# Performance work log

Hardware: AMD Instinct MI355X
Metric: run time of the kernel (lower is better)

Reference implementation:

```python
import jax, jax.numpy as jnp
import numpy as np


def _pad_ones(x):
    # prepend a ones column: [B, d] -> [B, d+1]
    b = x.shape[0]
    return jnp.concatenate([jnp.ones((b, 1), dtype=x.dtype), x], axis=1)


def setup_inputs() -> dict:
    key = jax.random.key(0)
    kt, ka, kv = jax.random.split(key, 3)
    B, D = 128, 63
    return {
        "t": jax.random.normal(kt, (B, D), dtype=jnp.float32),
        "a": jax.random.normal(ka, (B, D), dtype=jnp.float32),
        "v": jax.random.normal(kv, (B, D), dtype=jnp.float32),
    }


def reference(t, a, v):
    # Faithful to: bmm(a1[:, :, None], v1[:, None, :]) -> [B, da+1, dv+1],
    # then reshape to [B, (da+1)(dv+1), 1] and bmm with t1[:, None, :],
    # then flatten. Equivalent to triple outer product with index order (a, v, t).
    ah = _pad_ones(a)   # [B, da+1]
    vh = _pad_ones(v)   # [B, dv+1]
    th = _pad_ones(t)   # [B, dt+1]
    fusion = jnp.einsum('bi,bj,bk->bijk', ah, vh, th)  # [B, da+1, dv+1, dt+1]
    return fusion.reshape(a.shape[0], -1)
```

## Files before the change

### kernel.cpp

```cpp
#include <hip/hip_runtime.h>


__global__ __launch_bounds__(256) void tensorFusion_kernel(
    const float* __restrict__ t,
    const float* __restrict__ a,
    const float* __restrict__ v,
    float* __restrict__ out)
{
    const int D = 63;
    const int bi = blockIdx.x;
    const int b  = bi >> 6;
    const int i  = bi & 63;

    __shared__ float vh[64];
    __shared__ float th[64];

    const int tid = threadIdx.x;
    if (tid < 64) {
        vh[tid] = (tid == 0) ? 1.0f : v[b * D + (tid - 1)];
        th[tid] = (tid == 0) ? 1.0f : t[b * D + (tid - 1)];
    }
    const float ai = (i == 0) ? 1.0f : a[b * D + (i - 1)];
    __syncthreads();

    float4* __restrict__ outp = reinterpret_cast<float4*>(out + (size_t)bi * 4096);

    #pragma unroll
    for (int pass = 0; pass < 4; ++pass) {
        const int idx = pass * 256 + tid;
        const int off = idx << 2;
        const int j   = off >> 6;
        const int k   = off & 63;
        const float s = ai * vh[j];
        float4 r;
        r.x = s * th[k + 0];
        r.y = s * th[k + 1];
        r.z = s * th[k + 2];
        r.w = s * th[k + 3];
        outp[idx] = r;
    }
}

extern "C" void kernel_launch(void* const* d_in, const int* in_sizes, int n_in,
                              void* d_out, int out_size, void* d_ws, size_t ws_size,
                              hipStream_t stream) {
    const float* t = (const float*)d_in[0];
    const float* a = (const float*)d_in[1];
    const float* v = (const float*)d_in[2];
    float* out = (float*)d_out;

    tensorFusion_kernel<<<dim3(128 * 64), dim3(256), 0, stream>>>(t, a, v, out);
}
```

Before: 25.95 us.

## Compute four a-rows per block with nontemporal vector stores

Each block now produces four consecutive i rows instead of one, so the grid shrinks fourfold and each shared-memory load of v and t is reused across four output rows. The t values are read as 128-bit vectors from shared memory, and outputs are written with nontemporal stores to avoid cache pollution on this write-only, 16 MB output. Fewer blocks reduce launch and setup overhead, though there is less parallelism to hide store latency.

```diff
diff --git a/kernel.cpp b/kernel.cpp
--- a/kernel.cpp
+++ b/kernel.cpp
@@ -1,5 +1,7 @@
 #include <hip/hip_runtime.h>
 
+
+typedef float f4 __attribute__((ext_vector_type(4)));
 
 __global__ __launch_bounds__(256) void tensorFusion_kernel(
     const float* __restrict__ t,
@@ -7,37 +9,42 @@
     const float* __restrict__ v,
     float* __restrict__ out)
 {
-    const int D = 63;
-    const int bi = blockIdx.x;
-    const int b  = bi >> 6;
-    const int i  = bi & 63;
+    const int D   = 63;
+    const int blk = blockIdx.x;
+    const int b   = blk >> 4;
+    const int i0  = (blk & 15) << 2;
 
     __shared__ float vh[64];
     __shared__ float th[64];
+    __shared__ float ah[64];
 
     const int tid = threadIdx.x;
     if (tid < 64) {
-        vh[tid] = (tid == 0) ? 1.0f : v[b * D + (tid - 1)];
-        th[tid] = (tid == 0) ? 1.0f : t[b * D + (tid - 1)];
+        vh[tid] = (tid == 0) ? 1.0f : v[b * D + tid - 1];
+        th[tid] = (tid == 0) ? 1.0f : t[b * D + tid - 1];
+        ah[tid] = (tid == 0) ? 1.0f : a[b * D + tid - 1];
     }
-    const float ai = (i == 0) ? 1.0f : a[b * D + (i - 1)];
     __syncthreads();
 
-    float4* __restrict__ outp = reinterpret_cast<float4*>(out + (size_t)bi * 4096);
+    const float a0 = ah[i0 + 0];
+    const float a1 = ah[i0 + 1];
+    const float a2 = ah[i0 + 2];
+    const float a3 = ah[i0 + 3];
+
+    const f4* __restrict__ th4 = reinterpret_cast<const f4*>(th);
+    f4* __restrict__ outp =
+        reinterpret_cast<f4*>(out) + ((size_t)b * 64 + i0) * 1024;
 
     #pragma unroll
     for (int pass = 0; pass < 4; ++pass) {
         const int idx = pass * 256 + tid;
-        const int off = idx << 2;
-        const int j   = off >> 6;
-        const int k   = off & 63;
-        const float s = ai * vh[j];
-        float4 r;
-        r.x = s * th[k + 0];
-        r.y = s * th[k + 1];
-        r.z = s * th[k + 2];
-        r.w = s * th[k + 3];
-        outp[idx] = r;
+        const float vj = vh[idx >> 4];
+        const f4    tk = th4[idx & 15];
+
+        __builtin_nontemporal_store((a0 * vj) * tk, &outp[0 * 1024 + idx]);
+        __builtin_nontemporal_store((a1 * vj) * tk, &outp[1 * 1024 + idx]);
+        __builtin_nontemporal_store((a2 * vj) * tk, &outp[2 * 1024 + idx]);
+        __builtin_nontemporal_store((a3 * vj) * tk, &outp[3 * 1024 + idx]);
     }
 }
 
@@ -49,5 +56,5 @@
     const float* v = (const float*)d_in[2];
     float* out = (float*)d_out;
 
-    tensorFusion_kernel<<<dim3(128 * 64), dim3(256), 0, stream>>>(t, a, v, out);
+    tensorFusion_kernel<<<dim3(128 * 16), dim3(256), 0, stream>>>(t, a, v, out);
 }
```

New measurement: 29.37 us. 1.13x slower.
